# Kernel optimization log

Hardware: AMD Instinct MI355X
Metric: run time of the kernel (lower is better)

## Reference

```python
import jax, jax.numpy as jnp
import numpy as np
import math

B, N, M, D = 8, 2048, 2048, 512

def setup_inputs() -> dict:
    key = jax.random.key(0)
    ks = jax.random.split(key, 12)
    s = 1.0 / math.sqrt(D)
    return {
        "query_xyz": jax.random.normal(ks[0], (B, N, 3), jnp.float32),
        "query_feat": jax.random.normal(ks[1], (B, N, D), jnp.float32),
        "key_xyz": jax.random.normal(ks[2], (B, M, 3), jnp.float32),
        "key_feat": jax.random.normal(ks[3], (B, M, D), jnp.float32),
        "Wq": jax.random.normal(ks[4], (D, D), jnp.float32) * s,
        "bq": jnp.zeros((D,), jnp.float32),
        "Wk": jax.random.normal(ks[5], (D, D), jnp.float32) * s,
        "bk": jnp.zeros((D,), jnp.float32),
        "Wv": jax.random.normal(ks[6], (D, D), jnp.float32) * s,
        "bv": jnp.zeros((D,), jnp.float32),
        "Wo": jax.random.normal(ks[7], (D, D), jnp.float32) * s,
        "bo": jnp.zeros((D,), jnp.float32),
        "ln_g": jnp.ones((D,), jnp.float32),
        "ln_b": jnp.zeros((D,), jnp.float32),
    }

def reference(query_xyz, query_feat, key_xyz, key_feat,
              Wq, bq, Wk, bk, Wv, bv, Wo, bo, ln_g, ln_b):
    d = query_feat.shape[-1]
    # projections (torch Linear: x @ W.T + b)
    Q = jnp.einsum('bnd,ed->bne', query_feat, Wq) + bq
    K = jnp.einsum('bmd,ed->bme', key_feat, Wk) + bk
    V = jnp.einsum('bmd,ed->bme', key_feat, Wv) + bv
    scores = jnp.einsum('bnd,bmd->bnm', Q, K) / jnp.sqrt(jnp.float32(d))
    # pairwise euclidean distance via (||q||^2 + ||k||^2 - 2 q.k), avoids BxNxMx3
    qn = jnp.sum(query_xyz * query_xyz, axis=-1)  # [B,N]
    kn = jnp.sum(key_xyz * key_xyz, axis=-1)      # [B,M]
    d2 = qn[:, :, None] + kn[:, None, :] - 2.0 * jnp.einsum('bnc,bmc->bnm', query_xyz, key_xyz)
    dist = jnp.sqrt(jnp.maximum(d2, 1e-12))
    # distance bias: log(exp(-2*dist) + 1e-8)
    scores = scores + jnp.log(jnp.exp(-dist * 2.0) + 1e-8)
    attn = jax.nn.softmax(scores, axis=-1)
    # dropout is identity in eval mode
    attended = jnp.einsum('bnm,bme->bne', attn, V)
    out = jnp.einsum('bne,fe->bnf', attended, Wo) + bo
    x = query_feat + out
    # LayerNorm (eps=1e-5)
    mu = jnp.mean(x, axis=-1, keepdims=True)
    var = jnp.mean((x - mu) ** 2, axis=-1, keepdims=True)
    return (x - mu) * jax.lax.rsqrt(var + 1e-5) * ln_g + ln_b
```

## Files before the change

### kernel.cpp

```cpp
#include <hip/hip_runtime.h>

typedef __attribute__((ext_vector_type(8))) short short8;
typedef __attribute__((ext_vector_type(8))) unsigned short us8;
typedef __attribute__((ext_vector_type(4))) unsigned short us4;
typedef __attribute__((ext_vector_type(4))) float f32x4;

__device__ __forceinline__ float bf2f(unsigned short h) {
  return __uint_as_float(((unsigned int)h) << 16);
}
__device__ __forceinline__ unsigned short f2bf(float f) {
  unsigned int u = __float_as_uint(f);
  u += 0x7FFF + ((u >> 16) & 1);
  return (unsigned short)(u >> 16);
}

__device__ __forceinline__ void gload16(const void* g, void* l) {
  __builtin_amdgcn_global_load_lds(
      (const __attribute__((address_space(1))) unsigned int*)g,
      (__attribute__((address_space(3))) unsigned int*)l, 16, 0, 0);
}

#define BM 128
#define BN 128
#define BK 32

struct EpiParams {
  const float* bias;
  const float* aux0;
  const float* aux1;
  const void*  aux2;
  long  saux;
  float scale;
};

template<int EPI>
__global__ __launch_bounds__(256)
void gemm_bt(const unsigned short* __restrict__ A, const unsigned short* __restrict__ B,
             void* __restrict__ Cout, int Kd, int lda, int ldb, int ldc,
             long sA, long sB, long sC, EpiParams ep)
{
  __shared__ __attribute__((aligned(16))) char smem[16384];
  char* Al = smem;
  char* Bl = smem + 8192;

  const int t    = threadIdx.x;
  const int lane = t & 63;
  const int wid  = t >> 6;
  const int wr   = wid >> 1;
  const int wc   = wid & 1;
  const int tr   = lane & 15;
  const int tg   = lane >> 4;

  const int bz    = blockIdx.z;
  const int rbase = blockIdx.y * BM;
  const int cbase = blockIdx.x * BN;

  const unsigned short* Ab = A + (long)bz * sA;
  const unsigned short* Bb = B + (long)bz * sB;
  const char* Asrc = (const char*)(Ab + (long)rbase * lda);
  const char* Bsrc = (const char*)(Bb + (long)cbase * ldb);
  const long lda_b = (long)lda * 2;
  const long ldb_b = (long)ldb * 2;

  f32x4 acc[4][4] = {};

  for (int k0 = 0; k0 < Kd; k0 += BK) {
#pragma unroll
    for (int it = 0; it < 2; ++it) {
      const int boff = (it * 4 + wid) * 1024 + lane * 16;
      const int r  = boff >> 6;
      const int cb = boff & 63;
      gload16(Asrc + (long)r * lda_b + (k0 * 2 + cb), Al + (it * 4 + wid) * 1024);
      gload16(Bsrc + (long)r * ldb_b + (k0 * 2 + cb), Bl + (it * 4 + wid) * 1024);
    }
    __syncthreads();

    short8 af[4], bf[4];
#pragma unroll
    for (int m = 0; m < 4; ++m)
      af[m] = *(const short8*)(Al + ((wr * 64 + m * 16 + tr) * 32 + tg * 8) * 2);
#pragma unroll
    for (int n = 0; n < 4; ++n)
      bf[n] = *(const short8*)(Bl + ((wc * 64 + n * 16 + tr) * 32 + tg * 8) * 2);
#pragma unroll
    for (int m = 0; m < 4; ++m)
#pragma unroll
      for (int n = 0; n < 4; ++n)
        acc[m][n] = __builtin_amdgcn_mfma_f32_16x16x32_bf16(af[m], bf[n], acc[m][n], 0, 0, 0);
    __syncthreads();
  }

  if (EPI == 0) {
    unsigned short* C = (unsigned short*)Cout + (long)bz * sC;
#pragma unroll
    for (int n = 0; n < 4; ++n) {
      const int col = cbase + wc * 64 + n * 16 + tr;
      const float bv = ep.bias ? ep.bias[col] : 0.f;
#pragma unroll
      for (int m = 0; m < 4; ++m) {
#pragma unroll
        for (int i = 0; i < 4; ++i) {
          const int row = rbase + wr * 64 + m * 16 + tg * 4 + i;
          C[(long)row * ldc + col] = f2bf(acc[m][n][i] + bv);
        }
      }
    }
  } else if (EPI == 4) {
    if (cbase < 512) {
      unsigned short* C = (unsigned short*)Cout;
#pragma unroll
      for (int n = 0; n < 4; ++n) {
        const int col = cbase + wc * 64 + n * 16 + tr;
        const float bv = ep.bias[col];
#pragma unroll
        for (int m = 0; m < 4; ++m) {
#pragma unroll
          for (int i = 0; i < 4; ++i) {
            const int row = rbase + wr * 64 + m * 16 + tg * 4 + i;
            C[(long)row * 512 + col] = f2bf(acc[m][n][i] + bv);
          }
        }
      }
    } else {
      unsigned short* C = (unsigned short*)ep.aux2;
#pragma unroll
      for (int n = 0; n < 4; ++n) {
        const int e  = cbase - 512 + wc * 64 + n * 16 + tr;
        const float bv = ep.aux1[e];
#pragma unroll
        for (int m = 0; m < 4; ++m) {
          const int row0 = rbase + wr * 64 + m * 16 + tg * 4;
          const int b  = row0 >> 11;
          const int ml = row0 & 2047;
          us4 v;
#pragma unroll
          for (int i = 0; i < 4; ++i) v[i] = f2bf(acc[m][n][i] + bv);
          *(us4*)(C + ((long)b * 512 + e) * 2048 + ml) = v;
        }
      }
    }
  } else {
    float* C = (float*)Cout;
    const float* qf = ep.aux0;
#pragma unroll
    for (int n = 0; n < 4; ++n) {
      const int col = cbase + wc * 64 + n * 16 + tr;
      const float bv = ep.bias ? ep.bias[col] : 0.f;
#pragma unroll
      for (int m = 0; m < 4; ++m) {
#pragma unroll
        for (int i = 0; i < 4; ++i) {
          const int row = rbase + wr * 64 + m * 16 + tg * 4 + i;
          C[(long)row * 512 + col] = acc[m][n][i] + bv + qf[(long)row * 512 + col];
        }
      }
    }
  }
}

template<int EPI>
__global__ __launch_bounds__(512, 2)
void gemm2(const unsigned short* __restrict__ A, const unsigned short* __restrict__ B,
           void* __restrict__ Cout, int Kd, int lda, int ldb, int ldc,
           long sA, long sB, long sC, int ntn, EpiParams ep)
{
  __shared__ __attribute__((aligned(16))) char smem[98304];

  const int t    = threadIdx.x;
  const int lane = t & 63;
  const int wid  = t >> 6;
  const int wr   = wid >> 2;
  const int wc   = wid & 3;
  const int tr   = lane & 15;
  const int tg   = lane >> 4;

  const int bz    = blockIdx.x;
  const int rbase = (blockIdx.y / ntn) * 128;
  const int cbase = (blockIdx.y % ntn) * 256;

  const long lda_b = (long)lda * 2;
  const long ldb_b = (long)ldb * 2;
  const char* Asrc = (const char*)(A + (long)bz * sA + (long)rbase * lda);
  const char* Bsrc = (const char*)(B + (long)bz * sB + (long)cbase * ldb);

  const int srow   = t >> 3;
  const int scol16 = (t & 7) ^ ((t >> 3) & 7);
  const char* gA[2];
  const char* gB[4];
#pragma unroll
  for (int c = 0; c < 2; ++c)
    gA[c] = Asrc + (long)(c * 64 + srow) * lda_b + scol16 * 16;
#pragma unroll
  for (int c = 0; c < 4; ++c)
    gB[c] = Bsrc + (long)(c * 64 + srow) * ldb_b + scol16 * 16;

  f32x4 acc[4][4] = {};
  const int NT = Kd >> 6;
  int slot = 0;

#pragma unroll
  for (int c = 0; c < 2; ++c) gload16(gA[c], smem + c * 8192 + wid * 1024);
#pragma unroll
  for (int c = 0; c < 4; ++c) gload16(gB[c], smem + 16384 + c * 8192 + wid * 1024);
  __syncthreads();

  for (int tk = 0; tk < NT; ++tk) {
    if (tk + 1 < NT) {
      const int so = (slot ^ 1) * 49152;
      const long adv = (long)(tk + 1) * 128;
#pragma unroll
      for (int c = 0; c < 2; ++c) gload16(gA[c] + adv, smem + so + c * 8192 + wid * 1024);
#pragma unroll
      for (int c = 0; c < 4; ++c) gload16(gB[c] + adv, smem + so + 16384 + c * 8192 + wid * 1024);
    }
    const char* As = smem + slot * 49152;
    const char* Bs = As + 16384;
    const int x7 = tr & 7;
#pragma unroll
    for (int ks = 0; ks < 2; ++ks) {
      const int coff = ((ks * 4 + tg) ^ x7) * 16;
      short8 af[4], bf[4];
#pragma unroll
      for (int m = 0; m < 4; ++m)
        af[m] = *(const short8*)(As + (wr * 64 + m * 16 + tr) * 128 + coff);
#pragma unroll
      for (int n = 0; n < 4; ++n)
        bf[n] = *(const short8*)(Bs + (wc * 64 + n * 16 + tr) * 128 + coff);
#pragma unroll
      for (int m = 0; m < 4; ++m)
#pragma unroll
        for (int n = 0; n < 4; ++n)
          acc[m][n] = __builtin_amdgcn_mfma_f32_16x16x32_bf16(af[m], bf[n], acc[m][n], 0, 0, 0);
    }
    __syncthreads();
    slot ^= 1;
  }

  if (EPI == 0) {
    unsigned short* C = (unsigned short*)Cout + (long)bz * sC;
    const float* ls = (const float*)ep.aux2 + (long)bz * 2048 + rbase + wr * 64;
#pragma unroll
    for (int m = 0; m < 4; ++m) {
      const f32x4 lv = *(const f32x4*)(ls + m * 16 + tg * 4);
      f32x4 inv;
#pragma unroll
      for (int i = 0; i < 4; ++i) inv[i] = 1.f / lv[i];
#pragma unroll
      for (int n = 0; n < 4; ++n) {
        const int col = cbase + wc * 64 + n * 16 + tr;
#pragma unroll
        for (int i = 0; i < 4; ++i) {
          const int row = rbase + wr * 64 + m * 16 + tg * 4 + i;
          C[(long)row * ldc + col] = f2bf(acc[m][n][i] * inv[i]);
        }
      }
    }
  } else {
    float* qs  = (float*)smem;
    float* ks2 = (float*)smem + 384;
    if (t < 128) {
      const float* q = ep.aux0 + (long)bz * ep.saux + (long)(rbase + t) * 3;
      qs[t * 3] = q[0]; qs[t * 3 + 1] = q[1]; qs[t * 3 + 2] = q[2];
    } else if (t < 384) {
      const int tt = t - 128;
      const float* k2 = ep.aux1 + (long)bz * ep.saux + (long)(cbase + tt) * 3;
      ks2[tt * 3] = k2[0]; ks2[tt * 3 + 1] = k2[1]; ks2[tt * 3 + 2] = k2[2];
    }
    __syncthreads();
    unsigned short* C = (unsigned short*)Cout + (long)bz * sC;
    float* lrow = (float*)ep.aux2 + (long)bz * 2048 + rbase;
    float ps[4][4];
#pragma unroll
    for (int m = 0; m < 4; ++m) {
#pragma unroll
      for (int i = 0; i < 4; ++i) {
        ps[m][i] = 0.f;
        const int rl = wr * 64 + m * 16 + tg * 4 + i;
        const float qx = qs[rl * 3], qy = qs[rl * 3 + 1], qz = qs[rl * 3 + 2];
#pragma unroll
        for (int n = 0; n < 4; ++n) {
          const int cl = wc * 64 + n * 16 + tr;
          const float dx = qx - ks2[cl * 3];
          const float dy = qy - ks2[cl * 3 + 1];
          const float dz = qz - ks2[cl * 3 + 2];
          const float d2 = dx * dx + dy * dy + dz * dz;
          const float d  = sqrtf(fmaxf(d2, 1e-12f));
          const float bias = fmaxf(-2.f * d, -18.420680743952367f);
          const float p = __expf(acc[m][n][i] * ep.scale + bias - 5.f);
          ps[m][i] += p;
          C[(long)(rbase + rl) * ldc + (cbase + cl)] = f2bf(p);
        }
      }
    }
#pragma unroll
    for (int off = 1; off <= 8; off <<= 1)
#pragma unroll
      for (int m = 0; m < 4; ++m)
#pragma unroll
        for (int i = 0; i < 4; ++i)
          ps[m][i] += __shfl_xor(ps[m][i], off, 64);
    if (tr == 0) {
#pragma unroll
      for (int m = 0; m < 4; ++m)
#pragma unroll
        for (int i = 0; i < 4; ++i)
          atomicAdd(&lrow[wr * 64 + m * 16 + tg * 4 + i], ps[m][i]);
    }
  }
}

__global__ __launch_bounds__(256)
void ln_rows(const float* __restrict__ X, const float* __restrict__ g,
             const float* __restrict__ b, float* __restrict__ O)
{
  const int row  = blockIdx.x * 4 + (threadIdx.x >> 6);
  const int lane = threadIdx.x & 63;
  const float* xp = X + (long)row * 512;

  f32x4 v0 = *(const f32x4*)(xp + lane * 4);
  f32x4 v1 = *(const f32x4*)(xp + 256 + lane * 4);

  float s = 0.f;
#pragma unroll
  for (int j = 0; j < 4; ++j) s += v0[j] + v1[j];
#pragma unroll
  for (int off = 32; off; off >>= 1) s += __shfl_xor(s, off, 64);
  const float mu = s * (1.f / 512.f);

  float vs = 0.f;
#pragma unroll
  for (int j = 0; j < 4; ++j) {
    float d0 = v0[j] - mu, d1 = v1[j] - mu;
    vs += d0 * d0 + d1 * d1;
  }
#pragma unroll
  for (int off = 32; off; off >>= 1) vs += __shfl_xor(vs, off, 64);
  const float r = rsqrtf(vs * (1.f / 512.f) + 1e-5f);

  f32x4 g0 = *(const f32x4*)(g + lane * 4);
  f32x4 g1 = *(const f32x4*)(g + 256 + lane * 4);
  f32x4 b0 = *(const f32x4*)(b + lane * 4);
  f32x4 b1 = *(const f32x4*)(b + 256 + lane * 4);

  f32x4 o0, o1;
#pragma unroll
  for (int j = 0; j < 4; ++j) {
    o0[j] = (v0[j] - mu) * r * g0[j] + b0[j];
    o1[j] = (v1[j] - mu) * r * g1[j] + b1[j];
  }
  float* op = O + (long)row * 512;
  *(f32x4*)(op + lane * 4) = o0;
  *(f32x4*)(op + 256 + lane * 4) = o1;
}

__global__ __launch_bounds__(256)
void cvt_feat(const float* __restrict__ a, const float* __restrict__ b,
              unsigned short* __restrict__ oa, unsigned short* __restrict__ ob)
{
  const float* src = blockIdx.y ? b : a;
  unsigned short* dst = blockIdx.y ? ob : oa;
  const long i = blockIdx.x * 256 + threadIdx.x;
  const f32x4* s = (const f32x4*)src;
  f32x4 x = s[i * 2];
  f32x4 y = s[i * 2 + 1];
  us8 o;
#pragma unroll
  for (int j = 0; j < 4; ++j) { o[j] = f2bf(x[j]); o[4 + j] = f2bf(y[j]); }
  *(us8*)(dst + i * 8) = o;
}

__global__ __launch_bounds__(256)
void cvt_w(const float* __restrict__ w0, const float* __restrict__ w1,
           const float* __restrict__ w2, const float* __restrict__ w3,
           unsigned short* __restrict__ dst)
{
  const float* src = blockIdx.y == 0 ? w0 : blockIdx.y == 1 ? w1 : blockIdx.y == 2 ? w2 : w3;
  unsigned short* d = dst + (long)blockIdx.y * 262144;
  const long i = blockIdx.x * 256 + threadIdx.x;
  const f32x4* s = (const f32x4*)src;
  f32x4 x = s[i * 2];
  f32x4 y = s[i * 2 + 1];
  us8 o;
#pragma unroll
  for (int j = 0; j < 4; ++j) { o[j] = f2bf(x[j]); o[4 + j] = f2bf(y[j]); }
  *(us8*)(d + i * 8) = o;
}

extern "C" void kernel_launch(void* const* d_in, const int* in_sizes, int n_in,
                              void* d_out, int out_size, void* d_ws, size_t ws_size,
                              hipStream_t stream)
{
  const float* qxyz  = (const float*)d_in[0];
  const float* qfeat = (const float*)d_in[1];
  const float* kxyz  = (const float*)d_in[2];
  const float* kfeat = (const float*)d_in[3];
  const float* Wq = (const float*)d_in[4];
  const float* bq = (const float*)d_in[5];
  const float* Wk = (const float*)d_in[6];
  const float* bk = (const float*)d_in[7];
  const float* Wv = (const float*)d_in[8];
  const float* bv = (const float*)d_in[9];
  const float* Wo = (const float*)d_in[10];
  const float* bo = (const float*)d_in[11];
  const float* lng = (const float*)d_in[12];
  const float* lnb = (const float*)d_in[13];

  const long SZ_FEAT = 16777216;
  char* ws = (char*)d_ws;
  if (ws_size < (size_t)153092096) return;

  unsigned short* XQ  = (unsigned short*)(ws);
  unsigned short* XK  = (unsigned short*)(ws + SZ_FEAT);
  unsigned short* QB  = (unsigned short*)(ws + 2 * SZ_FEAT);
  unsigned short* KB  = (unsigned short*)(ws + 3 * SZ_FEAT);
  unsigned short* VT  = (unsigned short*)(ws + 4 * SZ_FEAT);
  unsigned short* WQB = (unsigned short*)(ws + 5 * SZ_FEAT);
  unsigned short* WKB = WQB + 262144;
  unsigned short* WOB = WQB + 786432;
  unsigned short* SB  = (unsigned short*)(ws + 5 * SZ_FEAT + 2097152);
  unsigned short* ATT = QB;
  float* XRES = (float*)ws;
  float* LSUM = (float*)(ws + SZ_FEAT);

  cvt_feat<<<dim3(4096, 2), 256, 0, stream>>>(qfeat, kfeat, XQ, XK);
  cvt_w<<<dim3(128, 4), 256, 0, stream>>>(Wq, Wk, Wv, Wo, WQB);

  EpiParams e0{}; e0.bias = bq;
  gemm_bt<0><<<dim3(4, 128, 1), 256, 0, stream>>>(XQ, WQB, QB, 512, 512, 512, 512, 0, 0, 0, e0);
  EpiParams e1{}; e1.bias = bk; e1.aux1 = bv; e1.aux2 = VT;
  gemm_bt<4><<<dim3(8, 128, 1), 256, 0, stream>>>(XK, WKB, KB, 512, 512, 512, 512, 0, 0, 0, e1);

  hipMemsetAsync(LSUM, 0, 8 * 2048 * sizeof(float), stream);

  EpiParams es{}; es.aux0 = qxyz; es.aux1 = kxyz; es.aux2 = LSUM; es.saux = 2048 * 3;
  es.scale = 0.044194173824159216f;
  gemm2<2><<<dim3(8, 128), 512, 0, stream>>>(QB, KB, SB, 512, 512, 512, 2048,
                                             (long)2048 * 512, (long)2048 * 512,
                                             (long)2048 * 2048, 8, es);

  EpiParams ep{}; ep.aux2 = LSUM;
  gemm2<0><<<dim3(8, 32), 512, 0, stream>>>(SB, VT, ATT, 2048, 2048, 2048, 512,
                                            (long)2048 * 2048, (long)512 * 2048,
                                            (long)2048 * 512, 2, ep);

  EpiParams eo{}; eo.bias = bo; eo.aux0 = qfeat;
  gemm_bt<3><<<dim3(4, 128, 1), 256, 0, stream>>>(ATT, WOB, XRES, 512, 512, 512, 512, 0, 0, 0, eo);

  ln_rows<<<4096, 256, 0, stream>>>(XRES, lng, lnb, (float*)d_out);
}
```

Measured before the change: 261.5 us.

## Triple-buffer gemm2 LDS pipeline with explicit vmcnt waits and MFMA priority

Replaces the double-buffered global-to-LDS pipeline in gemm2 with a three-stage ring, prefetching two K-tiles ahead. Explicit s_waitcnt vmcnt counts and raw barriers take the place of __syncthreads, and s_setprio raises wave priority around the MFMA block. The aim is to hide more global load latency behind matrix math. In exchange, LDS grows to 144 KB and launch bounds drop to one block per CU, which lowers occupancy.

```diff
diff --git a/kernel.cpp b/kernel.cpp
--- a/kernel.cpp
+++ b/kernel.cpp
@@ -159,12 +159,12 @@
 }
 
 template<int EPI>
-__global__ __launch_bounds__(512, 2)
+__global__ __launch_bounds__(512, 1)
 void gemm2(const unsigned short* __restrict__ A, const unsigned short* __restrict__ B,
            void* __restrict__ Cout, int Kd, int lda, int ldb, int ldc,
            long sA, long sB, long sC, int ntn, EpiParams ep)
 {
-  __shared__ __attribute__((aligned(16))) char smem[98304];
+  __shared__ __attribute__((aligned(16))) char smem[147456];
 
   const int t    = threadIdx.x;
   const int lane = t & 63;
@@ -196,24 +196,36 @@
 
   f32x4 acc[4][4] = {};
   const int NT = Kd >> 6;
-  int slot = 0;
-
-#pragma unroll
-  for (int c = 0; c < 2; ++c) gload16(gA[c], smem + c * 8192 + wid * 1024);
-#pragma unroll
-  for (int c = 0; c < 4; ++c) gload16(gB[c], smem + 16384 + c * 8192 + wid * 1024);
-  __syncthreads();
-
+
+#define STAGE(TK, S)                                                          \
+  {                                                                           \
+    char* _b = smem + (S) * 49152;                                            \
+    const long _adv = (long)(TK) * 128;                                       \
+    _Pragma("unroll")                                                         \
+    for (int c = 0; c < 2; ++c)                                               \
+      gload16(gA[c] + _adv, _b + c * 8192 + wid * 1024);                      \
+    _Pragma("unroll")                                                         \
+    for (int c = 0; c < 4; ++c)                                               \
+      gload16(gB[c] + _adv, _b + 16384 + c * 8192 + wid * 1024);              \
+  }
+
+  STAGE(0, 0);
+  if (NT > 1) STAGE(1, 1);
+
+  int cur = 0;
   for (int tk = 0; tk < NT; ++tk) {
-    if (tk + 1 < NT) {
-      const int so = (slot ^ 1) * 49152;
-      const long adv = (long)(tk + 1) * 128;
-#pragma unroll
-      for (int c = 0; c < 2; ++c) gload16(gA[c] + adv, smem + so + c * 8192 + wid * 1024);
-#pragma unroll
-      for (int c = 0; c < 4; ++c) gload16(gB[c] + adv, smem + so + 16384 + c * 8192 + wid * 1024);
-    }
-    const char* As = smem + slot * 49152;
+    if (tk + 2 < NT) {
+      STAGE(tk + 2, (cur + 2) % 3);
+      asm volatile("s_waitcnt vmcnt(12)" ::: "memory");
+    } else if (tk + 1 < NT) {
+      asm volatile("s_waitcnt vmcnt(6)" ::: "memory");
+    } else {
+      asm volatile("s_waitcnt vmcnt(0)" ::: "memory");
+    }
+    __builtin_amdgcn_s_barrier();
+    asm volatile("" ::: "memory");
+
+    const char* As = smem + cur * 49152;
     const char* Bs = As + 16384;
     const int x7 = tr & 7;
 #pragma unroll
@@ -226,15 +238,19 @@
 #pragma unroll
       for (int n = 0; n < 4; ++n)
         bf[n] = *(const short8*)(Bs + (wc * 64 + n * 16 + tr) * 128 + coff);
+      __builtin_amdgcn_s_setprio(1);
 #pragma unroll
       for (int m = 0; m < 4; ++m)
 #pragma unroll
         for (int n = 0; n < 4; ++n)
           acc[m][n] = __builtin_amdgcn_mfma_f32_16x16x32_bf16(af[m], bf[n], acc[m][n], 0, 0, 0);
-    }
-    __syncthreads();
-    slot ^= 1;
-  }
+      __builtin_amdgcn_s_setprio(0);
+    }
+    asm volatile("" ::: "memory");
+    __builtin_amdgcn_s_barrier();
+    cur = cur == 2 ? 0 : cur + 1;
+  }
+#undef STAGE
 
   if (EPI == 0) {
     unsigned short* C = (unsigned short*)Cout + (long)bz * sC;
```

After: 262.6 us. About the same (+0.4%).
